# Kernel tuning notes

Measured on AMD Instinct MI355X. Metric: run time of the kernel, lower is better.

Reference implementation:

```python
import jax, jax.numpy as jnp
import numpy as np

EPS = 1e-5
COMMITMENT_WEIGHT = 1.0


def setup_inputs() -> dict:
    key = jax.random.key(0)
    k1, k2 = jax.random.split(key)
    x = jax.random.normal(k1, (4, 4096, 128), dtype=jnp.float32)
    codebook = jax.random.normal(k2, (8192, 128), dtype=jnp.float32)
    return {"x": x, "codebook": codebook}


def _layernorm(x):
    # LayerNorm over last dim, elementwise_affine=False, eps=1e-5
    mu = jnp.mean(x, axis=-1, keepdims=True)
    var = jnp.mean(jnp.square(x - mu), axis=-1, keepdims=True)
    return (x - mu) * jax.lax.rsqrt(var + EPS)


def reference(x, codebook):
    b, n, d = x.shape
    xn = _layernorm(x)                      # [b, n, d]
    flat = xn.reshape(b * n, d)             # [bn, d]
    x2 = jnp.sum(flat * flat, axis=-1, keepdims=True)          # [bn, 1]
    e2 = jnp.sum(codebook * codebook, axis=-1)                  # [K]
    dots = jnp.einsum('nd,kd->nk', flat, codebook)              # [bn, K]
    distances = x2 - 2.0 * dots + e2[None, :]                   # [bn, K]
    embed_ind = jnp.argmin(distances, axis=-1)                  # [bn]
    quantize = codebook[embed_ind].reshape(b, n, d)             # gather
    embed_ind = embed_ind.reshape(b, n)
    loss = jnp.mean(jnp.square(quantize - xn)) * COMMITMENT_WEIGHT
    # straight-through
    quantize_st = xn + jax.lax.stop_gradient(quantize - xn)
    return (quantize_st, embed_ind, loss)
```

## Files before the change

kernel.cpp:

```cpp
#include <hip/hip_runtime.h>
#include <hip/hip_fp16.h>
#include <math.h>

typedef _Float16 half8  __attribute__((ext_vector_type(8)));
typedef _Float16 half2v __attribute__((ext_vector_type(2)));
typedef float   floatx4 __attribute__((ext_vector_type(4)));

#define ROWS   16384
#define DIM    128
#define KCODES 8192
#define NSPLIT 8
#define MTILE  256
#define NT     64
#define SPLITK (KCODES / NSPLIT)
#define NCHUNK (SPLITK / NT)
#define LOSS_SCALE (1.0f / ((float)ROWS * (float)DIM))

__device__ __forceinline__ void async_copy16(const _Float16* src, _Float16* dst_lds) {
  __builtin_amdgcn_global_load_lds((const __attribute__((address_space(1))) void*)src,
                                   (__attribute__((address_space(3))) void*)dst_lds,
                                   16, 0, 0);
}

__global__ __launch_bounds__(256) void prep_codebook(
    const float* __restrict__ cb, _Float16* __restrict__ ehg,
    _Float16* __restrict__ elg, float* __restrict__ e2g,
    float* __restrict__ out_loss)
{
  int tid = threadIdx.x;
  if (blockIdx.x == 0 && tid == 0) *out_loss = 0.f;
  int L = tid & 63;
  int row = blockIdx.x * 4 + (tid >> 6);
  float2 v = ((const float2*)(cb + (size_t)row * DIM))[L];
  float s2 = v.x * v.x + v.y * v.y;
  #pragma unroll
  for (int m = 1; m < 64; m <<= 1) s2 += __shfl_xor(s2, m);
  if (L == 0) e2g[row] = -0.5f * s2;
  _Float16 h0 = (_Float16)v.x, h1 = (_Float16)v.y;
  half2v hi = {h0, h1};
  half2v lo = {(_Float16)(v.x - (float)h0), (_Float16)(v.y - (float)h1)};
  ((half2v*)(ehg + (size_t)row * DIM))[L] = hi;
  ((half2v*)(elg + (size_t)row * DIM))[L] = lo;
}

__global__ __launch_bounds__(256, 2) void argmin_kernel(
    const float* __restrict__ x, const _Float16* __restrict__ ehg,
    const _Float16* __restrict__ elg, const float* __restrict__ e2g,
    float* __restrict__ best_part, int* __restrict__ idx_part,
    float* __restrict__ x2g)
{
  __shared__ _Float16 ebuf[2][2][64][128];

  int tid = threadIdx.x;
  int w   = tid >> 6;
  int L   = tid & 63;
  int c   = L & 15;
  int q   = L >> 4;

  int bx = blockIdx.x;
  int mt = bx & 63;
  int ns = bx >> 6;
  int code0 = ns * SPLITK;

  int rowbase = mt * MTILE + w * 64;

  half8 ah[4][4], al[4][4];

  #pragma unroll
  for (int g = 0; g < 4; ++g) {
    const float* xr = x + (size_t)(rowbase + g * 16 + c) * DIM;
    float v[32];
    #pragma unroll
    for (int ks = 0; ks < 4; ++ks) {
      float4 p0 = *(const float4*)(xr + ks * 32 + q * 8);
      float4 p1 = *(const float4*)(xr + ks * 32 + q * 8 + 4);
      v[ks*8+0] = p0.x; v[ks*8+1] = p0.y; v[ks*8+2] = p0.z; v[ks*8+3] = p0.w;
      v[ks*8+4] = p1.x; v[ks*8+5] = p1.y; v[ks*8+6] = p1.z; v[ks*8+7] = p1.w;
    }
    float s = 0.f;
    #pragma unroll
    for (int i = 0; i < 32; ++i) s += v[i];
    s += __shfl_xor(s, 16); s += __shfl_xor(s, 32);
    float mu = s * (1.0f / 128.0f);
    float s2 = 0.f;
    #pragma unroll
    for (int i = 0; i < 32; ++i) { float d = v[i] - mu; s2 += d * d; }
    s2 += __shfl_xor(s2, 16); s2 += __shfl_xor(s2, 32);
    float rstd = 1.0f / sqrtf(s2 * (1.0f / 128.0f) + 1e-5f);
    float x2 = 0.f;
    #pragma unroll
    for (int ks = 0; ks < 4; ++ks)
      #pragma unroll
      for (int j = 0; j < 8; ++j) {
        float xv = (v[ks*8+j] - mu) * rstd;
        x2 += xv * xv;
        _Float16 h = (_Float16)xv;
        ah[g][ks][j] = h;
        al[g][ks][j] = (_Float16)(xv - (float)h);
      }
    x2 += __shfl_xor(x2, 16); x2 += __shfl_xor(x2, 32);
    if (ns == 0 && q == 0) x2g[rowbase + g * 16 + c] = x2;
  }

  float best[4][4]; int bidx[4][4];
  #pragma unroll
  for (int g = 0; g < 4; ++g)
    #pragma unroll
    for (int r = 0; r < 4; ++r) { best[g][r] = -3.4e38f; bidx[g][r] = 0; }

  _Float16* lbase = &ebuf[0][0][0][0];

  auto stage = [&](int ch, int p) {
    int cbase = code0 + ch * NT;
    _Float16* lb = lbase + (size_t)p * 2 * 64 * 128;
    #pragma unroll
    for (int it = 0; it < 8; ++it) {
      int cid = it * 256 + tid;
      int arr = cid >> 10;
      int lc  = cid & 1023;
      int n   = lc >> 4;
      int kcs = lc & 15;
      int kc  = kcs ^ (n & 7);
      const _Float16* g = (arr ? elg : ehg) + (size_t)(cbase + n) * DIM + kc * 8;
      async_copy16(g, lb + (size_t)cid * 8);
    }
  };

  float e2n[4];
  #pragma unroll
  for (int s = 0; s < 4; ++s) e2n[s] = e2g[code0 + s * 16 + c];

  stage(0, 0);
  __syncthreads();

  for (int ch = 0; ch < NCHUNK; ++ch) {
    int p = ch & 1;
    int cbase = code0 + ch * NT;
    if (ch + 1 < NCHUNK) stage(ch + 1, p ^ 1);

    float e2h[4];
    #pragma unroll
    for (int s = 0; s < 4; ++s) e2h[s] = e2n[s];
    if (ch + 1 < NCHUNK) {
      #pragma unroll
      for (int s = 0; s < 4; ++s) e2n[s] = e2g[cbase + NT + s * 16 + c];
    }

    #pragma unroll
    for (int s = 0; s < 4; ++s) {
      int n = s * 16 + c;
      half8 bh[4], bl[4];
      #pragma unroll
      for (int ks = 0; ks < 4; ++ks) {
        int slot = ((ks * 4 + q) ^ (c & 7)) * 8;
        bh[ks] = *(const half8*)&ebuf[p][0][n][slot];
        bl[ks] = *(const half8*)&ebuf[p][1][n][slot];
      }
      int nn = cbase + n;
      #pragma unroll
      for (int g = 0; g < 4; ++g) {
        floatx4 acc = {e2h[s], e2h[s], e2h[s], e2h[s]};
        #pragma unroll
        for (int ks = 0; ks < 4; ++ks) {
          acc = __builtin_amdgcn_mfma_f32_16x16x32_f16(ah[g][ks], bh[ks], acc, 0, 0, 0);
          acc = __builtin_amdgcn_mfma_f32_16x16x32_f16(ah[g][ks], bl[ks], acc, 0, 0, 0);
          acc = __builtin_amdgcn_mfma_f32_16x16x32_f16(al[g][ks], bh[ks], acc, 0, 0, 0);
        }
        #pragma unroll
        for (int r = 0; r < 4; ++r) {
          float t = acc[r];
          if (t > best[g][r]) { best[g][r] = t; bidx[g][r] = nn; }
        }
      }
    }
    __syncthreads();
  }

  #pragma unroll
  for (int m = 1; m < 16; m <<= 1)
    #pragma unroll
    for (int g = 0; g < 4; ++g)
      #pragma unroll
      for (int r = 0; r < 4; ++r) {
        float ob = __shfl_xor(best[g][r], m);
        int   oi = __shfl_xor(bidx[g][r], m);
        if (ob > best[g][r] || (ob == best[g][r] && oi < bidx[g][r])) {
          best[g][r] = ob; bidx[g][r] = oi;
        }
      }
  if (c == 0) {
    #pragma unroll
    for (int g = 0; g < 4; ++g)
      #pragma unroll
      for (int r = 0; r < 4; ++r) {
        int row = rowbase + g * 16 + q * 4 + r;
        best_part[(size_t)row * NSPLIT + ns] = best[g][r];
        idx_part [(size_t)row * NSPLIT + ns] = bidx[g][r];
      }
  }
}

__global__ __launch_bounds__(256) void gather_loss_kernel(
    const float* __restrict__ cb, const float* __restrict__ best_part,
    const int* __restrict__ idx_part, const float* __restrict__ x2g,
    float* __restrict__ out_q, float* __restrict__ out_ind,
    float* __restrict__ out_loss)
{
  __shared__ int   sidx[32];
  __shared__ float sloss[32];
  int tid = threadIdx.x;
  int rb = blockIdx.x * 32;
  int r = tid >> 3, k = tid & 7;
  int row = rb + r;

  float b  = best_part[(size_t)row * NSPLIT + k];
  int   bi = idx_part [(size_t)row * NSPLIT + k];
  #pragma unroll
  for (int m = 1; m < 8; m <<= 1) {
    float ob = __shfl_xor(b, m);
    int   oi = __shfl_xor(bi, m);
    if (ob > b || (ob == b && oi < bi)) { b = ob; bi = oi; }
  }
  if (k == 0) {
    sidx[r] = bi;
    out_ind[row] = (float)bi;
    sloss[r] = x2g[row] - 2.0f * b;
  }
  __syncthreads();

  if (tid < 32) {
    float sl = sloss[tid];
    #pragma unroll
    for (int m = 1; m < 32; m <<= 1) sl += __shfl_xor(sl, m);
    if (tid == 0) atomicAdd(out_loss, sl * LOSS_SCALE);
  }

  const float4* cb4 = (const float4*)cb;
  float4* oq4 = (float4*)out_q;
  #pragma unroll
  for (int it = 0; it < 4; ++it) {
    int idx = it * 256 + tid;
    int r2 = idx >> 5, c4 = idx & 31;
    oq4[(size_t)(rb + r2) * 32 + c4] = cb4[(size_t)sidx[r2] * 32 + c4];
  }
}

extern "C" void kernel_launch(void* const* d_in, const int* in_sizes, int n_in,
                              void* d_out, int out_size, void* d_ws, size_t ws_size,
                              hipStream_t stream)
{
  const float* x  = (const float*)d_in[0];
  const float* cb = (const float*)d_in[1];

  char* ws = (char*)d_ws;
  _Float16* ehg      = (_Float16*)(ws + 0);
  _Float16* elg      = (_Float16*)(ws + 2097152);
  float*    e2g      = (float*)   (ws + 4194304);
  float*    best_part= (float*)   (ws + 4227072);
  int*      idx_part = (int*)     (ws + 4751360);
  float*    x2g      = (float*)   (ws + 5275648);

  float* out_q    = (float*)d_out;
  float* out_ind  = out_q + (size_t)ROWS * DIM;
  float* out_loss = out_ind + ROWS;

  prep_codebook<<<KCODES / 4, 256, 0, stream>>>(cb, ehg, elg, e2g, out_loss);
  argmin_kernel<<<(ROWS / MTILE) * NSPLIT, 256, 0, stream>>>(x, ehg, elg, e2g, best_part, idx_part, x2g);
  gather_loss_kernel<<<ROWS / 32, 256, 0, stream>>>(cb, best_part, idx_part, x2g, out_q, out_ind, out_loss);
}
```

Baseline: 162.6 us.

## Double block to 512 threads sharing codebook stage, precompute staging addresses

Each argmin block now runs 512 threads covering 512 rows, so every staged codebook chunk in LDS is reused by twice as many rows, and the grid shrinks to 256 blocks. The hi and lo fp16 codebook halves are packed into one buffer so staging addresses are a single base plus precomputed offsets. The chunk loop is unrolled by two so the LDS buffer index is a compile-time constant. The trade-off is fewer blocks (one per CU, launch bounds 512,1) and more threads waiting at each barrier, which may reduce latency hiding.

```diff
diff --git a/kernel.cpp b/kernel.cpp
--- a/kernel.cpp
+++ b/kernel.cpp
@@ -10,7 +10,7 @@
 #define DIM    128
 #define KCODES 8192
 #define NSPLIT 8
-#define MTILE  256
+#define MTILE  512
 #define NT     64
 #define SPLITK (KCODES / NSPLIT)
 #define NCHUNK (SPLITK / NT)
@@ -23,9 +23,8 @@
 }
 
 __global__ __launch_bounds__(256) void prep_codebook(
-    const float* __restrict__ cb, _Float16* __restrict__ ehg,
-    _Float16* __restrict__ elg, float* __restrict__ e2g,
-    float* __restrict__ out_loss)
+    const float* __restrict__ cb, _Float16* __restrict__ ehl,
+    float* __restrict__ e2g, float* __restrict__ out_loss)
 {
   int tid = threadIdx.x;
   if (blockIdx.x == 0 && tid == 0) *out_loss = 0.f;
@@ -39,17 +38,16 @@
   _Float16 h0 = (_Float16)v.x, h1 = (_Float16)v.y;
   half2v hi = {h0, h1};
   half2v lo = {(_Float16)(v.x - (float)h0), (_Float16)(v.y - (float)h1)};
-  ((half2v*)(ehg + (size_t)row * DIM))[L] = hi;
-  ((half2v*)(elg + (size_t)row * DIM))[L] = lo;
-}
-
-__global__ __launch_bounds__(256, 2) void argmin_kernel(
-    const float* __restrict__ x, const _Float16* __restrict__ ehg,
-    const _Float16* __restrict__ elg, const float* __restrict__ e2g,
-    float* __restrict__ best_part, int* __restrict__ idx_part,
-    float* __restrict__ x2g)
-{
-  __shared__ _Float16 ebuf[2][2][64][128];
+  ((half2v*)(ehl + (size_t)row * DIM))[L] = hi;
+  ((half2v*)(ehl + (size_t)(KCODES + row) * DIM))[L] = lo;
+}
+
+__global__ __launch_bounds__(512, 1) void argmin_kernel(
+    const float* __restrict__ x, const _Float16* __restrict__ ehl,
+    const float* __restrict__ e2g, float* __restrict__ best_part,
+    int* __restrict__ idx_part, float* __restrict__ x2g)
+{
+  __shared__ _Float16 ebuf[2 * 16384];
 
   int tid = threadIdx.x;
   int w   = tid >> 6;
@@ -58,14 +56,40 @@
   int q   = L >> 4;
 
   int bx = blockIdx.x;
-  int mt = bx & 63;
-  int ns = bx >> 6;
+  int mt = bx & 31;
+  int ns = bx >> 5;
   int code0 = ns * SPLITK;
 
   int rowbase = mt * MTILE + w * 64;
 
+  int loff[4], lsoff[4];
+  #pragma unroll
+  for (int it = 0; it < 4; ++it) {
+    int cid = it * 512 + tid;
+    int arr = cid >> 10;
+    int lc  = cid & 1023;
+    int n   = lc >> 4;
+    int kcs = lc & 15;
+    int kc  = kcs ^ (n & 7);
+    loff[it]  = arr * (KCODES * DIM) + n * DIM + kc * 8;
+    lsoff[it] = cid * 8;
+  }
+  int baddr[4][4];
+  #pragma unroll
+  for (int s = 0; s < 4; ++s)
+    #pragma unroll
+    for (int ks = 0; ks < 4; ++ks)
+      baddr[s][ks] = (s * 16 + c) * 128 + (((ks * 4 + q) ^ (c & 7)) * 8);
+
+  auto stage = [&](int ch, int p) {
+    int scal = (code0 + ch * NT) * DIM;
+    _Float16* lb = ebuf + p * 16384;
+    #pragma unroll
+    for (int it = 0; it < 4; ++it)
+      async_copy16(ehl + (scal + loff[it]), lb + lsoff[it]);
+  };
+
   half8 ah[4][4], al[4][4];
-
   #pragma unroll
   for (int g = 0; g < 4; ++g) {
     const float* xr = x + (size_t)(rowbase + g * 16 + c) * DIM;
@@ -108,72 +132,57 @@
     #pragma unroll
     for (int r = 0; r < 4; ++r) { best[g][r] = -3.4e38f; bidx[g][r] = 0; }
 
-  _Float16* lbase = &ebuf[0][0][0][0];
-
-  auto stage = [&](int ch, int p) {
-    int cbase = code0 + ch * NT;
-    _Float16* lb = lbase + (size_t)p * 2 * 64 * 128;
-    #pragma unroll
-    for (int it = 0; it < 8; ++it) {
-      int cid = it * 256 + tid;
-      int arr = cid >> 10;
-      int lc  = cid & 1023;
-      int n   = lc >> 4;
-      int kcs = lc & 15;
-      int kc  = kcs ^ (n & 7);
-      const _Float16* g = (arr ? elg : ehg) + (size_t)(cbase + n) * DIM + kc * 8;
-      async_copy16(g, lb + (size_t)cid * 8);
-    }
-  };
-
+  const float* e2p = e2g + code0 + c;
   float e2n[4];
   #pragma unroll
-  for (int s = 0; s < 4; ++s) e2n[s] = e2g[code0 + s * 16 + c];
+  for (int s = 0; s < 4; ++s) e2n[s] = e2p[s * 16];
 
   stage(0, 0);
   __syncthreads();
 
-  for (int ch = 0; ch < NCHUNK; ++ch) {
-    int p = ch & 1;
-    int cbase = code0 + ch * NT;
-    if (ch + 1 < NCHUNK) stage(ch + 1, p ^ 1);
-
-    float e2h[4];
-    #pragma unroll
-    for (int s = 0; s < 4; ++s) e2h[s] = e2n[s];
-    if (ch + 1 < NCHUNK) {
-      #pragma unroll
-      for (int s = 0; s < 4; ++s) e2n[s] = e2g[cbase + NT + s * 16 + c];
-    }
-
-    #pragma unroll
-    for (int s = 0; s < 4; ++s) {
-      int n = s * 16 + c;
-      half8 bh[4], bl[4];
-      #pragma unroll
-      for (int ks = 0; ks < 4; ++ks) {
-        int slot = ((ks * 4 + q) ^ (c & 7)) * 8;
-        bh[ks] = *(const half8*)&ebuf[p][0][n][slot];
-        bl[ks] = *(const half8*)&ebuf[p][1][n][slot];
-      }
-      int nn = cbase + n;
-      #pragma unroll
-      for (int g = 0; g < 4; ++g) {
-        floatx4 acc = {e2h[s], e2h[s], e2h[s], e2h[s]};
+  #pragma unroll 1
+  for (int ch2 = 0; ch2 < NCHUNK; ch2 += 2) {
+    #pragma unroll
+    for (int half = 0; half < 2; ++half) {
+      int ch = ch2 + half;
+      if (ch + 1 < NCHUNK) stage(ch + 1, half ^ 1);
+
+      float e2h[4];
+      #pragma unroll
+      for (int s = 0; s < 4; ++s) e2h[s] = e2n[s];
+      if (ch + 1 < NCHUNK) {
+        #pragma unroll
+        for (int s = 0; s < 4; ++s) e2n[s] = e2p[(ch + 1) * NT + s * 16];
+      }
+
+      #pragma unroll
+      for (int s = 0; s < 4; ++s) {
+        half8 bh[4], bl[4];
         #pragma unroll
         for (int ks = 0; ks < 4; ++ks) {
-          acc = __builtin_amdgcn_mfma_f32_16x16x32_f16(ah[g][ks], bh[ks], acc, 0, 0, 0);
-          acc = __builtin_amdgcn_mfma_f32_16x16x32_f16(ah[g][ks], bl[ks], acc, 0, 0, 0);
-          acc = __builtin_amdgcn_mfma_f32_16x16x32_f16(al[g][ks], bh[ks], acc, 0, 0, 0);
+          const _Float16* ba = ebuf + half * 16384 + baddr[s][ks];
+          bh[ks] = *(const half8*)ba;
+          bl[ks] = *(const half8*)(ba + 8192);
         }
+        int nn = code0 + ch * NT + s * 16 + c;
         #pragma unroll
-        for (int r = 0; r < 4; ++r) {
-          float t = acc[r];
-          if (t > best[g][r]) { best[g][r] = t; bidx[g][r] = nn; }
+        for (int g = 0; g < 4; ++g) {
+          floatx4 acc = {e2h[s], e2h[s], e2h[s], e2h[s]};
+          #pragma unroll
+          for (int ks = 0; ks < 4; ++ks) {
+            acc = __builtin_amdgcn_mfma_f32_16x16x32_f16(ah[g][ks], bh[ks], acc, 0, 0, 0);
+            acc = __builtin_amdgcn_mfma_f32_16x16x32_f16(ah[g][ks], bl[ks], acc, 0, 0, 0);
+            acc = __builtin_amdgcn_mfma_f32_16x16x32_f16(al[g][ks], bh[ks], acc, 0, 0, 0);
+          }
+          #pragma unroll
+          for (int r = 0; r < 4; ++r) {
+            float t = acc[r];
+            if (t > best[g][r]) { best[g][r] = t; bidx[g][r] = nn; }
+          }
         }
       }
+      __syncthreads();
     }
-    __syncthreads();
   }
 
   #pragma unroll
@@ -253,8 +262,7 @@
   const float* cb = (const float*)d_in[1];
 
   char* ws = (char*)d_ws;
-  _Float16* ehg      = (_Float16*)(ws + 0);
-  _Float16* elg      = (_Float16*)(ws + 2097152);
+  _Float16* ehl      = (_Float16*)(ws + 0);
   float*    e2g      = (float*)   (ws + 4194304);
   float*    best_part= (float*)   (ws + 4227072);
   int*      idx_part = (int*)     (ws + 4751360);
@@ -264,7 +272,7 @@
   float* out_ind  = out_q + (size_t)ROWS * DIM;
   float* out_loss = out_ind + ROWS;
 
-  prep_codebook<<<KCODES / 4, 256, 0, stream>>>(cb, ehg, elg, e2g, out_loss);
-  argmin_kernel<<<(ROWS / MTILE) * NSPLIT, 256, 0, stream>>>(x, ehg, elg, e2g, best_part, idx_part, x2g);
+  prep_codebook<<<KCODES / 4, 256, 0, stream>>>(cb, ehl, e2g, out_loss);
+  argmin_kernel<<<(ROWS / MTILE) * NSPLIT, 512, 0, stream>>>(x, ehl, e2g, best_part, idx_part, x2g);
   gather_loss_kernel<<<ROWS / 32, 256, 0, stream>>>(cb, best_part, idx_part, x2g, out_q, out_ind, out_loss);
 }
```

Result: slower. 203.0 us (+24.9%).
